# Kernel tuning notes

Measured on AMD Instinct MI355X. Metric: run time of the kernel, lower is better.

The kernel has to match this reference:

```python
import jax, jax.numpy as jnp
import numpy as np
import math

IN_C = 1024
OUT_C = 1024
HEADS = 16
GROUPS = 4

def grouped_linear(src, weight, bias):
    # src: [..., in_c]; weight: [g, in_c//g, out_c//g]; bias: [out_c]
    g, icg, ocg = weight.shape
    lead = src.shape[:-1]
    s = src.reshape(*lead, g, icg)
    out = jnp.einsum('...gi,gio->...go', s, weight)
    out = out.reshape(*lead, g * ocg)
    return out + bias

def restricted_softmax(src, margin=0.0):
    src_max = jnp.maximum(jnp.max(src, axis=-1, keepdims=True), 0.0)
    out = jnp.exp(src - src_max)
    return out / (jnp.sum(out, axis=-1, keepdims=True) + jnp.exp(margin - src_max))

def setup_inputs() -> dict:
    key = jax.random.key(0)
    ks = jax.random.split(key, 9)
    B, S = 2, 2048
    icg, ocg = IN_C // GROUPS, OUT_C // GROUPS
    scale = 1.0 / math.sqrt(icg)
    return {
        'query': jax.random.normal(ks[0], (B, S, IN_C), jnp.float32),
        'key': jax.random.normal(ks[1], (B, S, IN_C), jnp.float32),
        'value': jax.random.normal(ks[2], (B, S, IN_C), jnp.float32),
        'wq': jax.random.uniform(ks[3], (GROUPS, icg, ocg), jnp.float32, -scale, scale),
        'wk': jax.random.uniform(ks[4], (GROUPS, icg, ocg), jnp.float32, -scale, scale),
        'wv': jax.random.uniform(ks[5], (GROUPS, icg, ocg), jnp.float32, -scale, scale),
        'bq': jax.random.uniform(ks[6], (OUT_C,), jnp.float32, -scale, scale),
        'bk': jax.random.uniform(ks[7], (OUT_C,), jnp.float32, -scale, scale),
        'bv': jax.random.uniform(ks[8], (OUT_C,), jnp.float32, -scale, scale),
    }

def reference(query, key, value, wq, wk, wv, bq, bk, bv):
    q = grouped_linear(query, wq, bq)   # [B,S,OUT_C]
    k = grouped_linear(key, wk, bk)
    v = grouped_linear(value, wv, bv)
    B, Sq, _ = q.shape
    Sk = k.shape[-2]
    d = OUT_C // HEADS
    q = q.reshape(B, Sq, HEADS, d).transpose(0, 2, 1, 3)  # [B,H,Sq,d]
    k = k.reshape(B, Sk, HEADS, d).transpose(0, 2, 1, 3)
    v = v.reshape(B, Sk, HEADS, d).transpose(0, 2, 1, 3)
    score = jnp.einsum('bhqd,bhkd->bhqk', q, k) / math.sqrt(d)
    attn = restricted_softmax(score)
    out = jnp.einsum('bhqk,bhkd->bhqd', attn, v)
    out = out.transpose(0, 2, 1, 3).reshape(B, Sq, OUT_C)
    return out
```

## Files before the change

### kernel.cpp

```cpp
#include <hip/hip_runtime.h>
#include <hip/hip_bf16.h>

#define BB 2
#define SS 2048
#define CC 1024
#define HH 16
#define DDIM 64
#define NROWS (BB*SS)

#define QSC 0.18033688011112042f

typedef __attribute__((ext_vector_type(8))) short bf16x8;
typedef __attribute__((ext_vector_type(4))) float f32x4;

__device__ __forceinline__ f32x4 mfma16(bf16x8 a, bf16x8 b, f32x4 c) {
    return __builtin_amdgcn_mfma_f32_16x16x32_bf16(a, b, c, 0, 0, 0);
}

__global__ __launch_bounds__(256) void prep_wt(
    const float* __restrict__ wq, const float* __restrict__ wk,
    const float* __restrict__ wv, __hip_bfloat16* __restrict__ wt)
{
    const float* w = blockIdx.z == 0 ? wq : blockIdx.z == 1 ? wk : wv;
    const int g  = blockIdx.y;
    const int kt = blockIdx.x >> 2;
    const int nt = blockIdx.x & 3;
    __shared__ __hip_bfloat16 Ls[64][72];
    const int t = threadIdx.x;
    #pragma unroll
    for (int j = 0; j < 4; ++j) {
        int f4 = t + j*256;
        int row = f4 >> 4, n0 = (f4 & 15) * 4;
        float4 f = *(const float4*)&w[(size_t)g*65536 + (size_t)(kt*64+row)*256
                                      + nt*64 + n0];
        Ls[n0+0][row] = __float2bfloat16(f.x);
        Ls[n0+1][row] = __float2bfloat16(f.y);
        Ls[n0+2][row] = __float2bfloat16(f.z);
        Ls[n0+3][row] = __float2bfloat16(f.w);
    }
    __syncthreads();
    #pragma unroll
    for (int j = 0; j < 2; ++j) {
        int u = t + j*256;
        int nr = u >> 3, k8 = (u & 7) * 8;
        *(uint4*)&wt[((size_t)(blockIdx.z*4 + g)*256 + nt*64 + nr)*256
                     + kt*64 + k8] = *(const uint4*)&Ls[nr][k8];
    }
}

__global__ __launch_bounds__(256, 3) void proj_mfma(
    const float* __restrict__ qin, const float* __restrict__ kin,
    const float* __restrict__ vin,
    const __hip_bfloat16* __restrict__ wt,
    const float* __restrict__ bq, const float* __restrict__ bk,
    const float* __restrict__ bv,
    __hip_bfloat16* __restrict__ qs, __hip_bfloat16* __restrict__ ks_,
    __hip_bfloat16* __restrict__ vs)
{
    const int z = blockIdx.z;
    const float* src; const float* bias;
    if (z == 0)      { src = qin; bias = bq; }
    else if (z == 1) { src = kin; bias = bk; }
    else             { src = vin; bias = bv; }

    const int hp   = blockIdx.y;
    const int g    = hp >> 1;
    const int col0 = (hp & 1) * 128;
    const int row0 = blockIdx.x * 128;
    const int b    = row0 >> 11;
    const int s0   = row0 & 2047;

    __shared__ char smem[36864];
    auto As = (__hip_bfloat16 (*)[72])smem;
    auto Ws = (__hip_bfloat16 (*)[72])(smem + 18432);

    const int t    = threadIdx.x;
    const int wid  = t >> 6;
    const int lane = t & 63;
    const int l16  = lane & 15;
    const int quad = lane >> 4;

    f32x4 acc[2][8];
    #pragma unroll
    for (int mt = 0; mt < 2; ++mt)
        #pragma unroll
        for (int nt = 0; nt < 8; ++nt) acc[mt][nt] = (f32x4){0.f,0.f,0.f,0.f};

    const __hip_bfloat16* wtz = wt + (size_t)(z*4 + g)*65536;

    for (int kt = 0; kt < 4; ++kt) {
        __syncthreads();
        #pragma unroll
        for (int j = 0; j < 8; ++j) {
            int idx = t + j*256;
            int row = idx >> 4, c4 = (idx & 15) * 4;
            float4 f = *(const float4*)&src[(size_t)(row0 + row)*CC + g*256
                                            + kt*64 + c4];
            union { __hip_bfloat16 hh[4]; uint2 u; } pk;
            pk.hh[0] = __float2bfloat16(f.x); pk.hh[1] = __float2bfloat16(f.y);
            pk.hh[2] = __float2bfloat16(f.z); pk.hh[3] = __float2bfloat16(f.w);
            *(uint2*)&As[row][c4] = pk.u;
        }
        #pragma unroll
        for (int j = 0; j < 4; ++j) {
            int idx = t + j*256;
            int n = idx >> 3, k8 = (idx & 7) * 8;
            *(uint4*)&Ws[n][k8] =
                *(const uint4*)&wtz[(size_t)(col0 + n)*256 + kt*64 + k8];
        }
        __syncthreads();
        #pragma unroll
        for (int kss = 0; kss < 2; ++kss) {
            bf16x8 af[2], wf[8];
            #pragma unroll
            for (int mt = 0; mt < 2; ++mt)
                af[mt] = *(const bf16x8*)&As[wid*32 + mt*16 + l16][kss*32 + quad*8];
            #pragma unroll
            for (int nt = 0; nt < 8; ++nt)
                wf[nt] = *(const bf16x8*)&Ws[nt*16 + l16][kss*32 + quad*8];
            #pragma unroll
            for (int mt = 0; mt < 2; ++mt)
                #pragma unroll
                for (int nt = 0; nt < 8; ++nt)
                    acc[mt][nt] = mfma16(af[mt], wf[nt], acc[mt][nt]);
        }
    }

    float bval[8];
    #pragma unroll
    for (int nt = 0; nt < 8; ++nt) bval[nt] = bias[g*256 + col0 + nt*16 + l16];

    __syncthreads();

    if (z < 2) {
        const float scale = (z == 0) ? QSC : 1.0f;
        auto Ot = (__hip_bfloat16 (*)[136])smem;
        #pragma unroll
        for (int mt = 0; mt < 2; ++mt)
            #pragma unroll
            for (int nt = 0; nt < 8; ++nt)
                #pragma unroll
                for (int r = 0; r < 4; ++r)
                    Ot[wid*32 + mt*16 + quad*4 + r][nt*16 + l16] =
                        __float2bfloat16((acc[mt][nt][r] + bval[nt]) * scale);
        __syncthreads();
        __hip_bfloat16* base = (z == 0) ? qs : ks_;
        #pragma unroll
        for (int j = 0; j < 8; ++j) {
            int f = wid + j*4;
            int hl = f >> 4, t16l = (f >> 1) & 7, kcs = f & 1;
            uint4 v = *(const uint4*)&Ot[t16l*16 + l16][hl*64 + kcs*32 + quad*8];
            int h = hp*2 + hl;
            int t16g = (s0 >> 4) + t16l;
            *(uint4*)&base[((size_t)(b*HH + h) << 17)
                           + ((size_t)(t16g*2 + kcs) << 9) + lane*8] = v;
        }
    } else {
        auto Vl = (__hip_bfloat16 (*)[136])smem;
        #pragma unroll
        for (int mt = 0; mt < 2; ++mt)
            #pragma unroll
            for (int nt = 0; nt < 8; ++nt) {
                union { __hip_bfloat16 hh[4]; uint2 u; } pk;
                #pragma unroll
                for (int r = 0; r < 4; ++r)
                    pk.hh[r] = __float2bfloat16(acc[mt][nt][r] + bval[nt]);
                *(uint2*)&Vl[nt*16 + l16][wid*32 + mt*16 + quad*4] = pk.u;
            }
        __syncthreads();
        const int kc0 = s0 >> 5;
        #pragma unroll
        for (int j = 0; j < 8; ++j) {
            int f = wid + j*4;
            int hl = f >> 4, dt = (f >> 2) & 3, kcl = f & 3;
            uint4 v = *(const uint4*)&Vl[hl*64 + dt*16 + l16][kcl*32 + quad*8];
            int h = hp*2 + hl;
            *(uint4*)&vs[((size_t)(b*HH + h) << 17)
                         + ((size_t)(dt*64 + kc0 + kcl) << 9) + lane*8] = v;
        }
    }
}

__global__ __launch_bounds__(256, 2) void attn_mfma(
    const __hip_bfloat16* __restrict__ qs, const __hip_bfloat16* __restrict__ ks_,
    const __hip_bfloat16* __restrict__ vs, float* __restrict__ out)
{
    const int qt = blockIdx.x;
    const int h  = blockIdx.y;
    const int b  = blockIdx.z;

    __shared__ __hip_bfloat16 Ps[4][64][72];
    __shared__ float Uls[2][64][68];
    __shared__ float Lls[2][64];

    const int t    = threadIdx.x;
    const int wid  = t >> 6;
    const int qsub = wid & 1;
    const int kh   = wid >> 1;
    const int lane = t & 63;
    const int l16  = lane & 15;
    const int quad = lane >> 4;

    const __hip_bfloat16* qb = qs + ((size_t)(b*HH + h) << 17);
    const __hip_bfloat16* kb = ks_ + ((size_t)(b*HH + h) << 17);
    const __hip_bfloat16* vb = vs + ((size_t)(b*HH + h) << 17);

    const bf16x8 onesv = (bf16x8){16256,16256,16256,16256,
                                  16256,16256,16256,16256};

    bf16x8 qf[4][2];
    #pragma unroll
    for (int mt = 0; mt < 4; ++mt)
        #pragma unroll
        for (int kss = 0; kss < 2; ++kss)
            qf[mt][kss] = *(const bf16x8*)(qb +
                ((size_t)((qt*8 + qsub*4 + mt)*2 + kss) << 9) + lane*8);

    f32x4 O[4][4];
    f32x4 Lfrag[4];
    #pragma unroll
    for (int mt = 0; mt < 4; ++mt) {
        Lfrag[mt] = (f32x4){0.f,0.f,0.f,0.f};
        #pragma unroll
        for (int dt = 0; dt < 4; ++dt) O[mt][dt] = (f32x4){0.f,0.f,0.f,0.f};
    }

    bf16x8 kf[4][2];
    #pragma unroll
    for (int nt = 0; nt < 4; ++nt)
        #pragma unroll
        for (int kss = 0; kss < 2; ++kss)
            kf[nt][kss] = *(const bf16x8*)(kb +
                ((size_t)((kh*64 + nt)*2 + kss) << 9) + lane*8);

    for (int kt = 0; kt < 16; ++kt) {
        bf16x8 vf[4][2];
        #pragma unroll
        for (int dt = 0; dt < 4; ++dt)
            #pragma unroll
            for (int kss = 0; kss < 2; ++kss)
                vf[dt][kss] = *(const bf16x8*)(vb +
                    ((size_t)(dt*64 + kh*32 + kt*2 + kss) << 9) + lane*8);

        #pragma unroll
        for (int nt = 0; nt < 4; ++nt) {
            f32x4 st[4];
            #pragma unroll
            for (int mt = 0; mt < 4; ++mt) {
                f32x4 z = (f32x4){0.f,0.f,0.f,0.f};
                z = mfma16(kf[nt][0], qf[mt][0], z);
                st[mt] = mfma16(kf[nt][1], qf[mt][1], z);
            }
            #pragma unroll
            for (int mt = 0; mt < 4; ++mt) {
                float2 e0, e1;
                e0.x = __builtin_amdgcn_exp2f(st[mt][0]);
                e0.y = __builtin_amdgcn_exp2f(st[mt][1]);
                e1.x = __builtin_amdgcn_exp2f(st[mt][2]);
                e1.y = __builtin_amdgcn_exp2f(st[mt][3]);
                union { __hip_bfloat162 h2[2]; uint2 u; } pk;
                pk.h2[0] = __float22bfloat162_rn(e0);
                pk.h2[1] = __float22bfloat162_rn(e1);
                *(uint2*)&Ps[wid][mt*16 + l16][nt*16 + quad*4] = pk.u;
            }
        }

        if (kt + 1 < 16) {
            #pragma unroll
            for (int nt = 0; nt < 4; ++nt)
                #pragma unroll
                for (int kss = 0; kss < 2; ++kss)
                    kf[nt][kss] = *(const bf16x8*)(kb +
                        ((size_t)((kh*64 + (kt+1)*4 + nt)*2 + kss) << 9) + lane*8);
        }

        #pragma unroll
        for (int kss = 0; kss < 2; ++kss) {
            bf16x8 pf[4];
            #pragma unroll
            for (int mt = 0; mt < 4; ++mt)
                pf[mt] = *(const bf16x8*)&Ps[wid][mt*16 + l16][kss*32 + quad*8];
            #pragma unroll
            for (int mt = 0; mt < 4; ++mt) {
                Lfrag[mt] = mfma16(onesv, pf[mt], Lfrag[mt]);
                #pragma unroll
                for (int dt = 0; dt < 4; ++dt)
                    O[mt][dt] = mfma16(vf[dt][kss], pf[mt], O[mt][dt]);
            }
        }
    }

    if (kh == 1) {
        #pragma unroll
        for (int mt = 0; mt < 4; ++mt) {
            if (quad == 0) Lls[qsub][mt*16 + l16] = Lfrag[mt][0];
            #pragma unroll
            for (int dt = 0; dt < 4; ++dt) {
                float4 u4;
                u4.x = O[mt][dt][0]; u4.y = O[mt][dt][1];
                u4.z = O[mt][dt][2]; u4.w = O[mt][dt][3];
                *(float4*)&Uls[qsub][mt*16 + l16][dt*16 + quad*4] = u4;
            }
        }
    }
    __syncthreads();
    if (kh == 0) {
        #pragma unroll
        for (int mt = 0; mt < 4; ++mt) {
            const float inv = 1.0f /
                (1.0f + Lfrag[mt][0] + Lls[qsub][mt*16 + l16]);
            const size_t row = (size_t)b*SS + qt*128 + qsub*64 + mt*16 + l16;
            #pragma unroll
            for (int dt = 0; dt < 4; ++dt) {
                float4 u4 = *(const float4*)&Uls[qsub][mt*16 + l16][dt*16 + quad*4];
                float4 o4;
                o4.x = (O[mt][dt][0] + u4.x) * inv;
                o4.y = (O[mt][dt][1] + u4.y) * inv;
                o4.z = (O[mt][dt][2] + u4.z) * inv;
                o4.w = (O[mt][dt][3] + u4.w) * inv;
                *(float4*)&out[row*CC + h*DDIM + dt*16 + quad*4] = o4;
            }
        }
    }
}

extern "C" void kernel_launch(void* const* d_in, const int* in_sizes, int n_in,
                              void* d_out, int out_size, void* d_ws, size_t ws_size,
                              hipStream_t stream) {
    (void)in_sizes; (void)n_in; (void)out_size; (void)ws_size;
    const float* qin = (const float*)d_in[0];
    const float* kin = (const float*)d_in[1];
    const float* vin = (const float*)d_in[2];
    const float* wq  = (const float*)d_in[3];
    const float* wk  = (const float*)d_in[4];
    const float* wv  = (const float*)d_in[5];
    const float* bq  = (const float*)d_in[6];
    const float* bk  = (const float*)d_in[7];
    const float* bv  = (const float*)d_in[8];

    char* w0 = (char*)d_ws;
    __hip_bfloat16* qs = (__hip_bfloat16*)(w0);
    __hip_bfloat16* ks = (__hip_bfloat16*)(w0 + 8388608);
    __hip_bfloat16* vs = (__hip_bfloat16*)(w0 + 16777216);
    __hip_bfloat16* wt = (__hip_bfloat16*)(w0 + 25165824);
    float* out = (float*)d_out;

    prep_wt<<<dim3(16, 4, 3), 256, 0, stream>>>(wq, wk, wv, wt);
    proj_mfma<<<dim3(32, 8, 3), 256, 0, stream>>>(
        qin, kin, vin, wt, bq, bk, bv, qs, ks, vs);
    attn_mfma<<<dim3(16, 16, 2), 256, 0, stream>>>(qs, ks, vs, out);
}
```

Measured before the change: 163.5 us.

## Split attention key range four ways per block with XCD-aware tile mapping

The attention kernel now handles 64 query rows per block, with all four waves splitting the key sequence four ways, where each wave previously covered a 64-row half and a key half. The grid grows to 1024 blocks and uses a 1D index remapped so that blocks sharing a batch-head land on the same XCD for L2 reuse. Shared memory is aliased between the P staging buffer and the reduction buffers to allow 4 blocks per CU. In exchange there is a two-stage cross-wave tree reduction with extra barriers, and K and V are reloaded by twice as many blocks.

```diff
diff --git a/kernel.cpp b/kernel.cpp
--- a/kernel.cpp
+++ b/kernel.cpp
@@ -181,29 +181,32 @@
     }
 }
 
-__global__ __launch_bounds__(256, 2) void attn_mfma(
+__global__ __launch_bounds__(256, 4) void attn_mfma(
     const __hip_bfloat16* __restrict__ qs, const __hip_bfloat16* __restrict__ ks_,
     const __hip_bfloat16* __restrict__ vs, float* __restrict__ out)
 {
-    const int qt = blockIdx.x;
-    const int h  = blockIdx.y;
-    const int b  = blockIdx.z;
-
-    __shared__ __hip_bfloat16 Ps[4][64][72];
-    __shared__ float Uls[2][64][68];
-    __shared__ float Lls[2][64];
+    const int d   = blockIdx.x;
+    const int xcd = d & 7;
+    const int s   = d >> 3;
+    const int qt  = s & 31;
+    const int bh  = (s >> 5) * 8 + xcd;
+    const int h   = bh & 15;
+    const int b   = bh >> 4;
+
+    __shared__ char smem[37376];
+    auto Ps = (__hip_bfloat16 (*)[64][72])smem;
+    auto Ub = (float (*)[64][68])smem;
+    float* Lb = (float*)(smem + 36864);
 
     const int t    = threadIdx.x;
     const int wid  = t >> 6;
-    const int qsub = wid & 1;
-    const int kh   = wid >> 1;
     const int lane = t & 63;
     const int l16  = lane & 15;
     const int quad = lane >> 4;
 
-    const __hip_bfloat16* qb = qs + ((size_t)(b*HH + h) << 17);
-    const __hip_bfloat16* kb = ks_ + ((size_t)(b*HH + h) << 17);
-    const __hip_bfloat16* vb = vs + ((size_t)(b*HH + h) << 17);
+    const __hip_bfloat16* qb = qs  + ((size_t)bh << 17);
+    const __hip_bfloat16* kb = ks_ + ((size_t)bh << 17);
+    const __hip_bfloat16* vb = vs  + ((size_t)bh << 17);
 
     const bf16x8 onesv = (bf16x8){16256,16256,16256,16256,
                                   16256,16256,16256,16256};
@@ -214,7 +217,7 @@
         #pragma unroll
         for (int kss = 0; kss < 2; ++kss)
             qf[mt][kss] = *(const bf16x8*)(qb +
-                ((size_t)((qt*8 + qsub*4 + mt)*2 + kss) << 9) + lane*8);
+                ((size_t)((qt*4 + mt)*2 + kss) << 9) + lane*8);
 
     f32x4 O[4][4];
     f32x4 Lfrag[4];
@@ -231,16 +234,16 @@
         #pragma unroll
         for (int kss = 0; kss < 2; ++kss)
             kf[nt][kss] = *(const bf16x8*)(kb +
-                ((size_t)((kh*64 + nt)*2 + kss) << 9) + lane*8);
-
-    for (int kt = 0; kt < 16; ++kt) {
+                ((size_t)((wid*32 + nt)*2 + kss) << 9) + lane*8);
+
+    for (int kt = 0; kt < 8; ++kt) {
         bf16x8 vf[4][2];
         #pragma unroll
         for (int dt = 0; dt < 4; ++dt)
             #pragma unroll
             for (int kss = 0; kss < 2; ++kss)
                 vf[dt][kss] = *(const bf16x8*)(vb +
-                    ((size_t)(dt*64 + kh*32 + kt*2 + kss) << 9) + lane*8);
+                    ((size_t)(dt*64 + wid*16 + kt*2 + kss) << 9) + lane*8);
 
         #pragma unroll
         for (int nt = 0; nt < 4; ++nt) {
@@ -265,13 +268,13 @@
             }
         }
 
-        if (kt + 1 < 16) {
+        if (kt + 1 < 8) {
             #pragma unroll
             for (int nt = 0; nt < 4; ++nt)
                 #pragma unroll
                 for (int kss = 0; kss < 2; ++kss)
                     kf[nt][kss] = *(const bf16x8*)(kb +
-                        ((size_t)((kh*64 + (kt+1)*4 + nt)*2 + kss) << 9) + lane*8);
+                        ((size_t)((wid*32 + (kt+1)*4 + nt)*2 + kss) << 9) + lane*8);
         }
 
         #pragma unroll
@@ -290,29 +293,58 @@
         }
     }
 
-    if (kh == 1) {
+    __syncthreads();
+    if (wid & 1) {
+        const int half = wid >> 1;
         #pragma unroll
         for (int mt = 0; mt < 4; ++mt) {
-            if (quad == 0) Lls[qsub][mt*16 + l16] = Lfrag[mt][0];
+            if (quad == 0) Lb[half*64 + mt*16 + l16] = Lfrag[mt][0];
             #pragma unroll
             for (int dt = 0; dt < 4; ++dt) {
                 float4 u4;
                 u4.x = O[mt][dt][0]; u4.y = O[mt][dt][1];
                 u4.z = O[mt][dt][2]; u4.w = O[mt][dt][3];
-                *(float4*)&Uls[qsub][mt*16 + l16][dt*16 + quad*4] = u4;
-            }
-        }
-    }
-    __syncthreads();
-    if (kh == 0) {
+                *(float4*)&Ub[half][mt*16 + l16][dt*16 + quad*4] = u4;
+            }
+        }
+    }
+    __syncthreads();
+    if (!(wid & 1)) {
+        const int half = wid >> 1;
+        #pragma unroll
+        for (int mt = 0; mt < 4; ++mt) {
+            Lfrag[mt][0] += Lb[half*64 + mt*16 + l16];
+            #pragma unroll
+            for (int dt = 0; dt < 4; ++dt) {
+                float4 u4 = *(const float4*)&Ub[half][mt*16 + l16][dt*16 + quad*4];
+                O[mt][dt][0] += u4.x; O[mt][dt][1] += u4.y;
+                O[mt][dt][2] += u4.z; O[mt][dt][3] += u4.w;
+            }
+        }
+    }
+    if (wid == 2) {
+        #pragma unroll
+        for (int mt = 0; mt < 4; ++mt) {
+            if (quad == 0) Lb[64 + mt*16 + l16] = Lfrag[mt][0];
+            #pragma unroll
+            for (int dt = 0; dt < 4; ++dt) {
+                float4 u4;
+                u4.x = O[mt][dt][0]; u4.y = O[mt][dt][1];
+                u4.z = O[mt][dt][2]; u4.w = O[mt][dt][3];
+                *(float4*)&Ub[1][mt*16 + l16][dt*16 + quad*4] = u4;
+            }
+        }
+    }
+    __syncthreads();
+    if (wid == 0) {
         #pragma unroll
         for (int mt = 0; mt < 4; ++mt) {
             const float inv = 1.0f /
-                (1.0f + Lfrag[mt][0] + Lls[qsub][mt*16 + l16]);
-            const size_t row = (size_t)b*SS + qt*128 + qsub*64 + mt*16 + l16;
+                (1.0f + Lfrag[mt][0] + Lb[64 + mt*16 + l16]);
+            const size_t row = (size_t)b*SS + qt*64 + mt*16 + l16;
             #pragma unroll
             for (int dt = 0; dt < 4; ++dt) {
-                float4 u4 = *(const float4*)&Uls[qsub][mt*16 + l16][dt*16 + quad*4];
+                float4 u4 = *(const float4*)&Ub[1][mt*16 + l16][dt*16 + quad*4];
                 float4 o4;
                 o4.x = (O[mt][dt][0] + u4.x) * inv;
                 o4.y = (O[mt][dt][1] + u4.y) * inv;
@@ -348,5 +380,5 @@
     prep_wt<<<dim3(16, 4, 3), 256, 0, stream>>>(wq, wk, wv, wt);
     proj_mfma<<<dim3(32, 8, 3), 256, 0, stream>>>(
         qin, kin, vin, wt, bq, bk, bv, qs, ks, vs);
-    attn_mfma<<<dim3(16, 16, 2), 256, 0, stream>>>(qs, ks, vs, out);
-}
+    attn_mfma<<<dim3(1024, 1, 1), 256, 0, stream>>>(qs, ks, vs, out);
+}
```

Result: slower. 332.6 us (+103.4%).
